# Performance work log

Hardware: AMD Instinct MI355X
Metric: run time of the kernel (lower is better)

The kernel has to match this reference:

```python
import jax, jax.numpy as jnp
import numpy as np

BS, N, H = 8, 2048, 512
NEG_INF = -1.0e9
LEAKY_SLOPE = 0.01  # torch nn.LeakyReLU default


def setup_inputs() -> dict:
    key = jax.random.key(0)
    ks = jax.random.split(key, 8)
    feats = jax.random.normal(ks[0], (BS, N, H), dtype=jnp.float32)
    # random 0/1 adjacency with self-loops so every row has >=1 neighbor
    adj = jax.random.randint(ks[1], (BS, N, N), 0, 2).astype(jnp.float32)
    adj = jnp.maximum(adj, jnp.eye(N, dtype=jnp.float32)[None])
    s = 1.0 / np.sqrt(H)
    return {
        "feats": feats,
        "adj_mat": adj,
        "fc_w": jax.random.normal(ks[2], (H, H), dtype=jnp.float32) * s,
        "fc_b": jax.random.normal(ks[3], (H,), dtype=jnp.float32) * s,
        "q_w": jax.random.normal(ks[4], (1, H), dtype=jnp.float32) * s,
        "q_b": jax.random.normal(ks[5], (1,), dtype=jnp.float32) * s,
        "k_w": jax.random.normal(ks[6], (1, H), dtype=jnp.float32) * s,
        "k_b": jax.random.normal(ks[7], (1,), dtype=jnp.float32) * s,
    }


def reference(feats, adj_mat, fc_w, fc_b, q_w, q_b, k_w, k_b):
    # feats: [bs, N, H]; torch Linear: x @ W.T + b
    feat_proj = jnp.einsum("bnh,oh->bno", feats, fc_w) + fc_b          # [bs, N, H]
    q = jnp.einsum("bnh,oh->bno", feat_proj, q_w) + q_b                # [bs, N, 1]
    k = jnp.einsum("bnh,oh->bno", feat_proj, k_w) + k_b                # [bs, N, 1]
    logits = q + jnp.swapaxes(k, 2, 1)                                 # [bs, N, N] broadcast add
    masked = logits + (1.0 - adj_mat) * NEG_INF
    masked = jnp.where(masked >= 0, masked, LEAKY_SLOPE * masked)      # LeakyReLU
    atten = jax.nn.softmax(masked, axis=-1)
    # dropout is identity in eval mode
    out = jnp.einsum("bnm,bmh->bnh", atten, feat_proj)
    return out + feats  # residual=True
```

## Files before the change

### kernel.cpp

```cpp
#include <hip/hip_runtime.h>
#include <hip/hip_bf16.h>
#include <cstdint>
#include <cstddef>

#define BSZ 8
#define NN 2048
#define HH 512
#define MROWS (BSZ * NN)
#define LOG2E 1.44269504088896f

typedef __attribute__((ext_vector_type(4))) float f32x4;
typedef __attribute__((ext_vector_type(8))) short short8;
typedef __attribute__((ext_vector_type(4))) unsigned short us4;
typedef __attribute__((ext_vector_type(4))) uint32_t u32x4;

#if __has_builtin(__builtin_amdgcn_exp2f)
#define EXP2(x) __builtin_amdgcn_exp2f(x)
#else
#define EXP2(x) __expf((x) * 0.69314718056f)
#endif

static __device__ __forceinline__ unsigned short f2bf(float f) {
    uint32_t u = __builtin_bit_cast(uint32_t, f);
    u += 0x7fffu + ((u >> 16) & 1u);
    return (unsigned short)(u >> 16);
}

static __device__ __forceinline__ void async16(const unsigned short* g, unsigned short* l) {
    __builtin_amdgcn_global_load_lds(
        (const __attribute__((address_space(1))) void*)g,
        (__attribute__((address_space(3))) void*)l, 16, 0, 0);
}

__global__ __launch_bounds__(256) void k1_kernel(
    const float* __restrict__ feats, const float* __restrict__ fc_w,
    const float* __restrict__ fc_b, const float* __restrict__ q_w,
    const float* __restrict__ k_w, const float* __restrict__ adj,
    unsigned short* __restrict__ fpT, unsigned char* __restrict__ maskb,
    float* __restrict__ qpart, float* __restrict__ kpart) {
    const int bid = blockIdx.x;
    const int tid = threadIdx.x;
    if (bid < 512) {
        __shared__ alignas(16) unsigned short As[128 * 32];
        __shared__ alignas(16) unsigned short Bs[128 * 32];
        __shared__ float qred[2][128], kred[2][128];
        const int wave = tid >> 6, lane = tid & 63;
        const int wi = wave >> 1, wj = wave & 1;
        const int n0 = (bid & 3) * 128;
        const int i0 = (bid >> 2) * 128;
        const int r0 = tid >> 3;
        const int c4 = (tid & 7) * 4;
        const int fro = (lane & 15) * 32 + (lane >> 4) * 8;
        f32x4 acc[4][4];
#pragma unroll
        for (int a = 0; a < 4; ++a)
#pragma unroll
            for (int c = 0; c < 4; ++c) acc[a][c] = (f32x4)(0.f);

        for (int k0 = 0; k0 < HH; k0 += 32) {
            __syncthreads();
#pragma unroll
            for (int m = 0; m < 4; ++m) {
                f32x4 av = *(const f32x4*)&feats[(size_t)(i0 + r0 + 32 * m) * HH + k0 + c4];
                f32x4 bv = *(const f32x4*)&fc_w[(size_t)(n0 + r0 + 32 * m) * HH + k0 + c4];
                us4 oa, ob;
#pragma unroll
                for (int c = 0; c < 4; ++c) { oa[c] = f2bf(av[c]); ob[c] = f2bf(bv[c]); }
                *(us4*)&As[(r0 + 32 * m) * 32 + c4] = oa;
                *(us4*)&Bs[(r0 + 32 * m) * 32 + c4] = ob;
            }
            __syncthreads();
            short8 af[4], bf[4];
#pragma unroll
            for (int t = 0; t < 4; ++t) af[t] = *(const short8*)&As[(wi * 64 + t * 16) * 32 + fro];
#pragma unroll
            for (int t = 0; t < 4; ++t) bf[t] = *(const short8*)&Bs[(wj * 64 + t * 16) * 32 + fro];
#pragma unroll
            for (int it = 0; it < 4; ++it)
#pragma unroll
                for (int jt = 0; jt < 4; ++jt)
                    acc[it][jt] = __builtin_amdgcn_mfma_f32_16x16x32_bf16(af[it], bf[jt], acc[it][jt], 0, 0, 0);
        }

        int colv[4]; float cbv[4], qwv[4], kwv[4];
#pragma unroll
        for (int jt = 0; jt < 4; ++jt) {
            colv[jt] = n0 + wj * 64 + jt * 16 + (lane & 15);
            cbv[jt] = fc_b[colv[jt]];
            qwv[jt] = q_w[colv[jt]];
            kwv[jt] = k_w[colv[jt]];
        }
        const int b = i0 >> 11;
        const int il = i0 & 2047;
#pragma unroll
        for (int jt = 0; jt < 4; ++jt) {
#pragma unroll
            for (int it = 0; it < 4; ++it) {
                const int rb = wi * 64 + it * 16 + ((lane >> 4) << 2);
                us4 o;
#pragma unroll
                for (int r = 0; r < 4; ++r) o[r] = f2bf(acc[it][jt][r] + cbv[jt]);
                *(us4*)(fpT + ((size_t)b * HH + colv[jt]) * NN + il + rb) = o;
            }
        }
#pragma unroll
        for (int it = 0; it < 4; ++it) {
#pragma unroll
            for (int r = 0; r < 4; ++r) {
                float pq = 0.f, pk = 0.f;
#pragma unroll
                for (int jt = 0; jt < 4; ++jt) {
                    float v = acc[it][jt][r] + cbv[jt];
                    pq += v * qwv[jt];
                    pk += v * kwv[jt];
                }
                for (int off = 1; off < 16; off <<= 1) {
                    pq += __shfl_xor(pq, off, 64);
                    pk += __shfl_xor(pk, off, 64);
                }
                if ((lane & 15) == 0) {
                    const int rr = wi * 64 + it * 16 + ((lane >> 4) << 2) + r;
                    qred[wj][rr] = pq;
                    kred[wj][rr] = pk;
                }
            }
        }
        __syncthreads();
        if (tid < 128) {
            const size_t o = (size_t)(n0 >> 7) * MROWS + i0 + tid;
            qpart[o] = qred[0][tid] + qred[1][tid];
            kpart[o] = kred[0][tid] + kred[1][tid];
        }
    } else {
        const int a = bid - 512;
        const int wave = tid >> 6, lane = tid & 63;
#pragma unroll
        for (int s = 0; s < 4; ++s) {
            const int row = a * 16 + s * 4 + wave;
            const float* ar = adj + (size_t)row * NN;
#pragma unroll
            for (int p = 0; p < 4; ++p) {
                f32x4 v0 = *(const f32x4*)&ar[p * 512 + lane * 8];
                f32x4 v1 = *(const f32x4*)&ar[p * 512 + lane * 8 + 4];
                float fb = v0[0] + 2.f * v0[1] + 4.f * v0[2] + 8.f * v0[3]
                         + 16.f * v1[0] + 32.f * v1[1] + 64.f * v1[2] + 128.f * v1[3];
                maskb[(size_t)row * 256 + p * 64 + lane] = (unsigned char)(unsigned int)fb;
            }
        }
    }
}

__global__ __launch_bounds__(256) void fused_pv_kernel(
    const unsigned short* __restrict__ fpT, const unsigned char* __restrict__ maskb,
    const float* __restrict__ qpart, const float* __restrict__ kpart,
    const float* __restrict__ q_b, const float* __restrict__ k_b,
    const float* __restrict__ feats, float* __restrict__ out) {
    __shared__ alignas(16) unsigned short As[64 * 32];
    __shared__ alignas(16) unsigned short Bs[256 * 32];
    __shared__ float kLDS[NN];
    __shared__ float qLDS[64];
    __shared__ float zfl[256];
    __shared__ float rzl[64];
    const int tid = threadIdx.x;
    const int wave = tid >> 6, lane = tid & 63;
    const int wi = wave >> 1, wj = wave & 1;
    const int bid = blockIdx.x;
    const int b = bid & 7;
    const int t6 = bid >> 3;
    const int i0 = (t6 >> 1) * 64;
    const int n0 = (t6 & 1) * 256;
    const size_t rowbase = (size_t)b * NN + i0;

    {
        const float kb = k_b[0], qb = q_b[0];
#pragma unroll
        for (int s = 0; s < 8; ++s) {
            const int j = s * 256 + tid;
            const size_t gj = (size_t)b * NN + j;
            kLDS[j] = (kpart[gj] + kpart[MROWS + gj] + kpart[2 * MROWS + gj]
                     + kpart[3 * MROWS + gj] + kb) * LOG2E;
        }
        if (tid < 64) {
            const size_t gi = rowbase + tid;
            qLDS[tid] = (qpart[gi] + qpart[MROWS + gi] + qpart[2 * MROWS + gi]
                       + qpart[3 * MROWS + gi] + qb) * LOG2E;
        }
    }
    __syncthreads();

    const int r0 = tid >> 2;
    const int c8 = (tid & 3) * 8;
    const float qi = qLDS[r0];
    float z = 0.f;

    const unsigned short* Bt = fpT + (size_t)b * HH * NN;
    const uint32_t* mk = (const uint32_t*)maskb;
    const size_t mrow = (rowbase + r0) * 64;
    const int lrow = lane >> 2, lseg = (lane & 3) * 8;
    const int fro = (lane & 15) * 32 + (lane >> 4) * 8;

    f32x4 acc[2][8];
#pragma unroll
    for (int a = 0; a < 2; ++a)
#pragma unroll
        for (int c = 0; c < 8; ++c) acc[a][c] = (f32x4)(0.f);

    uint32_t mcur = mk[mrow];
    for (int k0 = 0; k0 < NN; k0 += 32) {
        __syncthreads();
        {
            const int rbase = wave * 64;
            const unsigned short* gb = Bt + (size_t)(n0 + rbase + lrow) * NN + k0 + lseg;
            async16(gb, &Bs[rbase * 32]);
            async16(gb + (size_t)16 * NN, &Bs[(rbase + 16) * 32]);
            async16(gb + (size_t)32 * NN, &Bs[(rbase + 32) * 32]);
            async16(gb + (size_t)48 * NN, &Bs[(rbase + 48) * 32]);
        }
        uint32_t mnext = 0;
        if (k0 + 32 < NN) mnext = mk[mrow + ((k0 + 32) >> 5)];
        const f32x4 kv0 = *(const f32x4*)&kLDS[k0 + c8];
        const f32x4 kv1 = *(const f32x4*)&kLDS[k0 + c8 + 4];
        const uint32_t byte8 = (mcur >> c8) & 0xffu;
        float wv[8];
#pragma unroll
        for (int c = 0; c < 8; ++c) {
            float s = qi + (c < 4 ? kv0[c] : kv1[c - 4]);
            s = fmaxf(s, 0.01f * s);
            float e = EXP2(s);
            wv[c] = ((byte8 >> c) & 1u) ? e : 0.f;
            z += wv[c];
        }
        u32x4 pk;
#pragma unroll
        for (int p = 0; p < 4; ++p) {
            uint32_t lo = __builtin_bit_cast(uint32_t, wv[2 * p]) + 0x8000u;
            uint32_t hi = __builtin_bit_cast(uint32_t, wv[2 * p + 1]) + 0x8000u;
            pk[p] = __builtin_amdgcn_perm(hi, lo, 0x07060302u);
        }
        *(u32x4*)&As[r0 * 32 + c8] = pk;
        __syncthreads();
        short8 af[2], bf[8];
#pragma unroll
        for (int t = 0; t < 2; ++t) af[t] = *(const short8*)&As[(wi * 32 + t * 16) * 32 + fro];
#pragma unroll
        for (int t = 0; t < 8; ++t) bf[t] = *(const short8*)&Bs[(wj * 128 + t * 16) * 32 + fro];
#pragma unroll
        for (int it = 0; it < 2; ++it)
#pragma unroll
            for (int jt = 0; jt < 8; ++jt)
                acc[it][jt] = __builtin_amdgcn_mfma_f32_16x16x32_bf16(af[it], bf[jt], acc[it][jt], 0, 0, 0);
        mcur = mnext;
    }

    zfl[tid] = z;
    __syncthreads();
    if (tid < 64) {
        const float* zp = &zfl[tid * 4];
        rzl[tid] = 1.0f / (zp[0] + zp[1] + zp[2] + zp[3]);
    }
    __syncthreads();

#pragma unroll
    for (int it = 0; it < 2; ++it) {
        const int rb = wi * 32 + it * 16 + ((lane >> 4) << 2);
        float rv[4];
#pragma unroll
        for (int r = 0; r < 4; ++r) rv[r] = rzl[rb + r];
#pragma unroll
        for (int jt = 0; jt < 8; ++jt) {
            const int col = n0 + wj * 128 + jt * 16 + (lane & 15);
#pragma unroll
            for (int r = 0; r < 4; ++r) {
                const size_t idx = (rowbase + rb + r) * HH + col;
                out[idx] = acc[it][jt][r] * rv[r] + feats[idx];
            }
        }
    }
}

extern "C" void kernel_launch(void* const* d_in, const int* in_sizes, int n_in,
                              void* d_out, int out_size, void* d_ws, size_t ws_size,
                              hipStream_t stream) {
    const float* feats = (const float*)d_in[0];
    const float* adj   = (const float*)d_in[1];
    const float* fc_w  = (const float*)d_in[2];
    const float* fc_b  = (const float*)d_in[3];
    const float* q_w   = (const float*)d_in[4];
    const float* q_b   = (const float*)d_in[5];
    const float* k_w   = (const float*)d_in[6];
    const float* k_b   = (const float*)d_in[7];
    float* out = (float*)d_out;

    char* w = (char*)d_ws;
    auto alloc = [&](size_t bytes) {
        char* p = w;
        w += (bytes + 255) & ~(size_t)255;
        return p;
    };
    unsigned short* fpT   = (unsigned short*)alloc((size_t)BSZ * HH * NN * 2);
    unsigned char*  maskb = (unsigned char*)alloc((size_t)MROWS * 256);
    float* qpart = (float*)alloc((size_t)4 * MROWS * 4);
    float* kpart = (float*)alloc((size_t)4 * MROWS * 4);

    k1_kernel<<<512 + 1024, 256, 0, stream>>>(feats, fc_w, fc_b, q_w, k_w, adj,
                                              fpT, maskb, qpart, kpart);
    fused_pv_kernel<<<512, 256, 0, stream>>>(
        fpT, maskb, qpart, kpart, q_b, k_b, feats, out);
}
```

Baseline: 320.1 us.

## Pre-convert feats and fc_w to bf16 and stage GEMM tiles via async LDS loads

Result: no change. 323.9 us (+1.2%).

```diff
diff --git a/kernel.cpp b/kernel.cpp
--- a/kernel.cpp
+++ b/kernel.cpp
@@ -32,8 +32,38 @@
         (__attribute__((address_space(3))) void*)l, 16, 0, 0);
 }
 
-__global__ __launch_bounds__(256) void k1_kernel(
+__global__ __launch_bounds__(256) void prep_kernel(
     const float* __restrict__ feats, const float* __restrict__ fc_w,
+    unsigned short* __restrict__ feats_bf, unsigned short* __restrict__ fcw_bf) {
+    const int bid = blockIdx.x;
+    const int tid = threadIdx.x;
+    if (bid < 2048) {
+        const int base = bid * 1024 + tid;
+#pragma unroll
+        for (int j = 0; j < 4; ++j) {
+            const int i = base + j * 256;
+            f32x4 v = ((const f32x4*)feats)[i];
+            us4 o;
+#pragma unroll
+            for (int c = 0; c < 4; ++c) o[c] = f2bf(v[c]);
+            ((us4*)feats_bf)[i] = o;
+        }
+    } else {
+        const int base = (bid - 2048) * 1024 + tid;
+#pragma unroll
+        for (int j = 0; j < 4; ++j) {
+            const int i = base + j * 256;
+            f32x4 v = ((const f32x4*)fc_w)[i];
+            us4 o;
+#pragma unroll
+            for (int c = 0; c < 4; ++c) o[c] = f2bf(v[c]);
+            ((us4*)fcw_bf)[i] = o;
+        }
+    }
+}
+
+__global__ __launch_bounds__(256) void k2_kernel(
+    const unsigned short* __restrict__ A, const unsigned short* __restrict__ Bt,
     const float* __restrict__ fc_b, const float* __restrict__ q_w,
     const float* __restrict__ k_w, const float* __restrict__ adj,
     unsigned short* __restrict__ fpT, unsigned char* __restrict__ maskb,
@@ -48,8 +78,9 @@
         const int wi = wave >> 1, wj = wave & 1;
         const int n0 = (bid & 3) * 128;
         const int i0 = (bid >> 2) * 128;
-        const int r0 = tid >> 3;
-        const int c4 = (tid & 7) * 4;
+        const int K = HH;
+        const int lrow = lane >> 2;
+        const int lseg = (lane & 3) * 8;
         const int fro = (lane & 15) * 32 + (lane >> 4) * 8;
         f32x4 acc[4][4];
 #pragma unroll
@@ -57,17 +88,16 @@
 #pragma unroll
             for (int c = 0; c < 4; ++c) acc[a][c] = (f32x4)(0.f);
 
-        for (int k0 = 0; k0 < HH; k0 += 32) {
+        for (int k0 = 0; k0 < K; k0 += 32) {
             __syncthreads();
-#pragma unroll
-            for (int m = 0; m < 4; ++m) {
-                f32x4 av = *(const f32x4*)&feats[(size_t)(i0 + r0 + 32 * m) * HH + k0 + c4];
-                f32x4 bv = *(const f32x4*)&fc_w[(size_t)(n0 + r0 + 32 * m) * HH + k0 + c4];
-                us4 oa, ob;
-#pragma unroll
-                for (int c = 0; c < 4; ++c) { oa[c] = f2bf(av[c]); ob[c] = f2bf(bv[c]); }
-                *(us4*)&As[(r0 + 32 * m) * 32 + c4] = oa;
-                *(us4*)&Bs[(r0 + 32 * m) * 32 + c4] = ob;
+            {
+                const int c0 = wave * 2;
+                const unsigned short* ga = A + (size_t)(i0 + c0 * 16 + lrow) * K + k0 + lseg;
+                async16(ga, &As[(c0 * 16) * 32]);
+                async16(ga + (size_t)16 * K, &As[(c0 * 16 + 16) * 32]);
+                const unsigned short* gb = Bt + (size_t)(n0 + c0 * 16 + lrow) * K + k0 + lseg;
+                async16(gb, &Bs[(c0 * 16) * 32]);
+                async16(gb + (size_t)16 * K, &Bs[(c0 * 16 + 16) * 32]);
             }
             __syncthreads();
             short8 af[4], bf[4];
@@ -135,8 +165,8 @@
         const int a = bid - 512;
         const int wave = tid >> 6, lane = tid & 63;
 #pragma unroll
-        for (int s = 0; s < 4; ++s) {
-            const int row = a * 16 + s * 4 + wave;
+        for (int s = 0; s < 2; ++s) {
+            const int row = a * 8 + s * 4 + wave;
             const float* ar = adj + (size_t)row * NN;
 #pragma unroll
             for (int p = 0; p < 4; ++p) {
@@ -297,12 +327,15 @@
         w += (bytes + 255) & ~(size_t)255;
         return p;
     };
+    unsigned short* feats_bf = (unsigned short*)alloc((size_t)BSZ * NN * HH * 2);
+    unsigned short* fcw_bf   = (unsigned short*)alloc((size_t)HH * HH * 2);
     unsigned short* fpT   = (unsigned short*)alloc((size_t)BSZ * HH * NN * 2);
     unsigned char*  maskb = (unsigned char*)alloc((size_t)MROWS * 256);
     float* qpart = (float*)alloc((size_t)4 * MROWS * 4);
     float* kpart = (float*)alloc((size_t)4 * MROWS * 4);
 
-    k1_kernel<<<512 + 1024, 256, 0, stream>>>(feats, fc_w, fc_b, q_w, k_w, adj,
+    prep_kernel<<<2112, 256, 0, stream>>>(feats, fc_w, feats_bf, fcw_bf);
+    k2_kernel<<<512 + 2048, 256, 0, stream>>>(feats_bf, fcw_bf, fc_b, q_w, k_w, adj,
                                               fpT, maskb, qpart, kpart);
     fused_pv_kernel<<<512, 256, 0, stream>>>(
         fpT, maskb, qpart, kpart, q_b, k_b, feats, out);
```
